# Kernel optimization log

Measured on AMD Instinct MI355X. Metric: run time of the kernel, lower is better.

The kernel has to match this reference:

```python
import jax, jax.numpy as jnp
import numpy as np

N = 100000   # nodes
E = 1600000  # edges
D = 128      # state_dim
H1 = 512
H2 = 256


def setup_inputs() -> dict:
    key = jax.random.key(0)
    ks = jax.random.split(key, 8)
    x = jax.random.normal(ks[0], (N, D), jnp.float32)
    edge_index = jax.random.randint(ks[1], (2, E), 0, N, dtype=jnp.int64)
    W_gcn = jax.random.normal(ks[2], (D, D), jnp.float32) * (1.0 / np.sqrt(D))
    b_gcn = jnp.zeros((D,), jnp.float32)
    W1 = jax.random.normal(ks[3], (D, H1), jnp.float32) * (1.0 / np.sqrt(D))
    b1 = jnp.zeros((H1,), jnp.float32)
    W2 = jax.random.normal(ks[4], (H1, H2), jnp.float32) * (1.0 / np.sqrt(H1))
    b2 = jnp.zeros((H2,), jnp.float32)
    W3 = jax.random.normal(ks[5], (H2, 1), jnp.float32) * (1.0 / np.sqrt(H2))
    b3 = jnp.zeros((1,), jnp.float32)
    return {"x": x, "edge_index": edge_index, "W_gcn": W_gcn, "b_gcn": b_gcn,
            "W1": W1, "b1": b1, "W2": W2, "b2": b2, "W3": W3, "b3": b3}


def _gcn_conv(x, edge_index, W, b):
    # PyG GCNConv: linear transform, add self-loops, symmetric deg^-1/2 norm,
    # scatter-sum messages from src to dst, add bias.
    n = x.shape[0]
    loop = jnp.arange(n, dtype=edge_index.dtype)
    src = jnp.concatenate([edge_index[0], loop])
    dst = jnp.concatenate([edge_index[1], loop])
    deg = jax.ops.segment_sum(jnp.ones_like(dst, x.dtype), dst, num_segments=n)
    dinv = jnp.where(deg > 0, jax.lax.rsqrt(jnp.maximum(deg, 1e-12)), 0.0)
    norm = dinv[src] * dinv[dst]                      # [E+N]
    h = x @ W                                         # [N, D]
    msg = h[src] * norm[:, None]                      # gather + scale
    out = jax.ops.segment_sum(msg, dst, num_segments=n)  # scatter-add
    return out + b


def reference(x, edge_index, W_gcn, b_gcn, W1, b1, W2, b2, W3, b3):
    out = jax.nn.relu(_gcn_conv(x, edge_index, W_gcn, b_gcn))
    h = out + x                                       # residual
    h = jax.nn.relu(h @ W1 + b1)
    h = jax.nn.relu(h @ W2 + b2)                      # dropout is identity in eval
    return h @ W3 + b3                                # [N, 1]
```

## Files before the change

kernel.cpp:

```cpp
#include <hip/hip_runtime.h>

#define DN  128
#define H1N 512
#define H2N 256
#define TILE_A 4096
#define BKT_CAP 6144

typedef __attribute__((ext_vector_type(8))) short short8_t;
typedef __attribute__((ext_vector_type(4))) float f32x4;

__device__ inline ushort f2bf(float f) {
  union { float f; unsigned u; } v; v.f = f;
  unsigned r = v.u + 0x7FFF + ((v.u >> 16) & 1);
  return (ushort)(r >> 16);
}
__device__ inline float asf(unsigned u) {
  union { unsigned u; float f; } v; v.u = u;
  return v.f;
}


__global__ __launch_bounds__(256) void k_bucketA(const int* __restrict__ ei,
                                                 int* __restrict__ bcur,
                                                 uint* __restrict__ pairs,
                                                 int E, int NB) {
  __shared__ int hist[512];
  __shared__ int start[512];
  __shared__ int cur[512];
  __shared__ int gbase[512];
  __shared__ uint lp[TILE_A];
  __shared__ ushort bid[TILE_A];
  int t = threadIdx.x;
  int base = blockIdx.x * TILE_A;
  int cnt = E - base; if (cnt > TILE_A) cnt = TILE_A;

  for (int i = t; i < 512; i += 256) hist[i] = 0;
  __syncthreads();

  int sreg[16], dreg[16];
#pragma unroll
  for (int k = 0; k < 16; ++k) {
    int idx = t + 256 * k;
    bool v = idx < cnt;
    sreg[k] = v ? ei[base + idx] : 0;
    dreg[k] = v ? ei[E + base + idx] : -1;
    if (v) atomicAdd(&hist[dreg[k] >> 8], 1);
  }
  __syncthreads();

  for (int i = t; i < 512; i += 256) start[i] = hist[i];
  __syncthreads();
  for (int o = 1; o < 512; o <<= 1) {
    int i0 = t, i1 = t + 256;
    int v0 = (i0 >= o) ? start[i0 - o] : 0;
    int v1 = (i1 >= o) ? start[i1 - o] : 0;
    __syncthreads();
    start[i0] += v0;
    start[i1] += v1;
    __syncthreads();
  }
  for (int i = t; i < 512; i += 256) start[i] -= hist[i];
  __syncthreads();
  for (int i = t; i < 512; i += 256) cur[i] = start[i];
  __syncthreads();

#pragma unroll
  for (int k = 0; k < 16; ++k) {
    if (dreg[k] >= 0) {
      int d = dreg[k] >> 8;
      int p = atomicAdd(&cur[d], 1);
      lp[p]  = ((uint)sreg[k] << 8) | ((uint)dreg[k] & 255u);
      bid[p] = (ushort)d;
    }
  }
  __syncthreads();

  for (int i = t; i < NB; i += 256)
    gbase[i] = hist[i] ? atomicAdd(&bcur[i], hist[i]) : 0;
  __syncthreads();

  for (int p = t; p < cnt; p += 256) {
    int d = bid[p];
    int o = gbase[d] + (p - start[d]);
    if (o < BKT_CAP) pairs[(size_t)d * BKT_CAP + o] = lp[p];
  }
}


__global__ __launch_bounds__(256) void k_bucketB(const uint* __restrict__ pairs,
                                                 const int* __restrict__ bcur,
                                                 int* __restrict__ csr,
                                                 int* __restrict__ ro,
                                                 int* __restrict__ re,
                                                 float* __restrict__ dinv,
                                                 int N) {
  __shared__ int hist[256];
  __shared__ int cur[256];
  __shared__ int lout[BKT_CAP];
  __shared__ uint lp[BKT_CAP];
  int b = blockIdx.x, t = threadIdx.x;
  size_t p0 = (size_t)b * BKT_CAP;
  int cnt = bcur[b]; if (cnt > BKT_CAP) cnt = BKT_CAP;

  hist[t] = 0;
  __syncthreads();
  for (int k = t; k < cnt; k += 256) {
    uint pr = pairs[p0 + k];
    lp[k] = pr;
    atomicAdd(&hist[pr & 255u], 1);
  }
  __syncthreads();

  int v = hist[t];
  cur[t] = v; __syncthreads();
  for (int o = 1; o < 256; o <<= 1) {
    int a = (t >= o) ? cur[t - o] : 0;
    __syncthreads();
    cur[t] += a;
    __syncthreads();
  }
  int excl = cur[t] - v;
  int node = (b << 8) + t;
  if (node < N) {
    ro[node] = (int)p0 + excl;
    re[node] = (int)p0 + excl + v;
    dinv[node] = rsqrtf((float)(v + 1));
  }
  __syncthreads();
  cur[t] = excl;
  __syncthreads();

  for (int k = t; k < cnt; k += 256) {
    uint pr = lp[k];
    int p = atomicAdd(&cur[(int)(pr & 255u)], 1);
    lout[p] = (int)(pr >> 8);
  }
  __syncthreads();
  for (int k = t; k < cnt; k += 256) csr[p0 + k] = lout[k];
}


__device__ inline void pack_one(int idx, const float* __restrict__ W,
                                ushort* __restrict__ Wp, int K, int Ncols) {
  int ksn = K >> 5;
  int l  = idx & 63;
  int ks = (idx >> 6) % ksn;
  int ct = idx / (64 * ksn);
  int col = ct * 16 + (l & 15);
  int kb  = ks * 32 + (l >> 4) * 8;
  short8_t v;
#pragma unroll
  for (int r = 0; r < 8; ++r)
    v[r] = (short)f2bf(W[(size_t)(kb + r) * Ncols + col]);
  *(short8_t*)&Wp[(size_t)idx * 8] = v;
}

__global__ __launch_bounds__(256) void k_packall(const float* __restrict__ Wg,
                                                 const float* __restrict__ W1,
                                                 const float* __restrict__ W2,
                                                 ushort* __restrict__ Wgp,
                                                 ushort* __restrict__ W1p,
                                                 ushort* __restrict__ W2p) {
  int idx = blockIdx.x * 256 + threadIdx.x;
  if (idx < 2048)        pack_one(idx, Wg, Wgp, DN, DN);
  else if (idx < 10240)  pack_one(idx - 2048, W1, W1p, DN, H1N);
  else if (idx < 26624)  pack_one(idx - 10240, W2, W2p, H1N, H2N);
}


__global__ __launch_bounds__(256, 4) void k_gemm1(const float* __restrict__ x,
                                                  const ushort* __restrict__ Wgp,
                                                  const float* __restrict__ dinv,
                                                  ushort* __restrict__ hs,
                                                  ushort* __restrict__ xb, int N) {
  __shared__ ushort xT[64 * 128];
  int t = threadIdx.x;
  int row0 = blockIdx.x * 64;

#pragma unroll
  for (int i = 0; i < 4; ++i) {
    int c = t + 256 * i;
    int r = c >> 4, d0 = (c & 15) * 8;
    int gr = row0 + r;
    float4 v0 = {0,0,0,0}, v1 = {0,0,0,0};
    if (gr < N) {
      v0 = *(const float4*)(x + (size_t)gr * DN + d0);
      v1 = *(const float4*)(x + (size_t)gr * DN + d0 + 4);
    }
    short8_t p;
    p[0]=(short)f2bf(v0.x); p[1]=(short)f2bf(v0.y); p[2]=(short)f2bf(v0.z); p[3]=(short)f2bf(v0.w);
    p[4]=(short)f2bf(v1.x); p[5]=(short)f2bf(v1.y); p[6]=(short)f2bf(v1.z); p[7]=(short)f2bf(v1.w);
    if (gr < N) {
      int s = (c & 15) >> 1, half = (c & 15) & 1;
      *(short8_t*)(xb + ((size_t)s * N + gr) * 16 + half * 8) = p;
    }
    *(short8_t*)((char*)xT + r * 256 + ((d0 * 2) ^ ((r & 7) << 4))) = p;
  }
  __syncthreads();

  int w = t >> 6, l = t & 63;
  int lr = l & 15, lk = l >> 4;
  const short8_t* pbg = (const short8_t*)Wgp;

  f32x4 acc[4][2];
#pragma unroll
  for (int mf = 0; mf < 4; ++mf)
#pragma unroll
    for (int n = 0; n < 2; ++n) acc[mf][n] = (f32x4){0.f,0.f,0.f,0.f};

  auto g_load = [&](short8_t (&bb)[2], int ks) {
#pragma unroll
    for (int n = 0; n < 2; ++n)
      bb[n] = pbg[((w * 2 + n) * 4 + ks) * 64 + l];
  };
  auto g_mfma = [&](short8_t (&bb)[2], int ks) {
    short8_t a[4];
#pragma unroll
    for (int mf = 0; mf < 4; ++mf) {
      int r = mf * 16 + lr;
      a[mf] = *(const short8_t*)((const char*)xT + r * 256 + ((ks * 64 + lk * 16) ^ ((r & 7) << 4)));
    }
#pragma unroll
    for (int mf = 0; mf < 4; ++mf)
#pragma unroll
      for (int n = 0; n < 2; ++n)
        acc[mf][n] = __builtin_amdgcn_mfma_f32_16x16x32_bf16(a[mf], bb[n], acc[mf][n], 0, 0, 0);
  };

  short8_t bA[2], bB[2];
  g_load(bA, 0);
  g_load(bB, 1); g_mfma(bA, 0);
  g_load(bA, 2); g_mfma(bB, 1);
  g_load(bB, 3); g_mfma(bA, 2);
  g_mfma(bB, 3);

  float dv[4][4];
#pragma unroll
  for (int mf = 0; mf < 4; ++mf)
#pragma unroll
    for (int r2 = 0; r2 < 4; ++r2) {
      int gr = row0 + mf * 16 + lk * 4 + r2;
      dv[mf][r2] = (gr < N) ? dinv[gr] : 0.f;
    }
#pragma unroll
  for (int n = 0; n < 2; ++n) {
    int s = w * 2 + n;
#pragma unroll
    for (int mf = 0; mf < 4; ++mf)
#pragma unroll
      for (int r2 = 0; r2 < 4; ++r2) {
        int gr = row0 + mf * 16 + lk * 4 + r2;
        if (gr < N)
          hs[((size_t)s * N + gr) * 16 + lr] = f2bf(acc[mf][n][r2] * dv[mf][r2]);
      }
  }
}


__global__ __launch_bounds__(256) void k_agg(const ushort* __restrict__ hs,
                                             const ushort* __restrict__ xb,
                                             const int* __restrict__ csr,
                                             const int* __restrict__ ro,
                                             const int* __restrict__ re,
                                             const float* __restrict__ dinv,
                                             const float* __restrict__ bg,
                                             ushort* __restrict__ aggb, int N) {
  int t = threadIdx.x;
  int slice = blockIdx.x & 7;
  int node = (blockIdx.x >> 3) * 64 + (t >> 2);
  if (node >= N) return;
  int d0 = (t & 3) * 4;

  const ushort* hss = hs + (size_t)slice * N * 16;
  int beg = ro[node], end = re[node];
  float dn = dinv[node];
  uint2 selfv = *(const uint2*)(hss + (size_t)node * 16 + d0);
  uint2 xv    = *(const uint2*)(xb + ((size_t)slice * N + node) * 16 + d0);
  float4 bv   = *(const float4*)(bg + slice * 16 + d0);

  float s0 = 0.f, s1 = 0.f, s2 = 0.f, s3 = 0.f;
  auto accum = [&](uint2 v) {
    s0 += asf(v.x << 16); s1 += asf(v.x & 0xffff0000u);
    s2 += asf(v.y << 16); s3 += asf(v.y & 0xffff0000u);
  };

  int e = beg;
  for (; e + 4 <= end; e += 4) {
    int i0 = csr[e], i1 = csr[e + 1], i2 = csr[e + 2], i3 = csr[e + 3];
    uint2 v0 = *(const uint2*)(hss + (size_t)i0 * 16 + d0);
    uint2 v1 = *(const uint2*)(hss + (size_t)i1 * 16 + d0);
    uint2 v2 = *(const uint2*)(hss + (size_t)i2 * 16 + d0);
    uint2 v3 = *(const uint2*)(hss + (size_t)i3 * 16 + d0);
    accum(v0); accum(v1); accum(v2); accum(v3);
  }
  if (e + 2 <= end) {
    int i0 = csr[e], i1 = csr[e + 1];
    uint2 v0 = *(const uint2*)(hss + (size_t)i0 * 16 + d0);
    uint2 v1 = *(const uint2*)(hss + (size_t)i1 * 16 + d0);
    accum(v0); accum(v1);
    e += 2;
  }
  if (e < end) {
    int i0 = csr[e];
    accum(*(const uint2*)(hss + (size_t)i0 * 16 + d0));
  }
  accum(selfv);

  uint outp[2];
  {
    ushort lo = f2bf(fmaxf(s0 * dn + bv.x, 0.f) + asf(xv.x << 16));
    ushort hi = f2bf(fmaxf(s1 * dn + bv.y, 0.f) + asf(xv.x & 0xffff0000u));
    outp[0] = (uint)lo | ((uint)hi << 16);
    lo = f2bf(fmaxf(s2 * dn + bv.z, 0.f) + asf(xv.y << 16));
    hi = f2bf(fmaxf(s3 * dn + bv.w, 0.f) + asf(xv.y & 0xffff0000u));
    outp[1] = (uint)lo | ((uint)hi << 16);
  }
  *(uint2*)(aggb + ((size_t)slice * N + node) * 16 + d0) = *(uint2*)outp;
}


__global__ __launch_bounds__(512, 2) void k_mlp(const ushort* __restrict__ aggb,
                                                const ushort* __restrict__ W1p,
                                                const float* __restrict__ b1,
                                                const ushort* __restrict__ W2p,
                                                const float* __restrict__ b2,
                                                const float* __restrict__ W3,
                                                const float* __restrict__ b3,
                                                float* __restrict__ out, int N) {
  __shared__ ushort aT[64 * 128];
  __shared__ ushort t1[64 * 512];
  int t = threadIdx.x;
  int row0 = blockIdx.x * 64;

#pragma unroll
  for (int i = 0; i < 2; ++i) {
    int u = t + 512 * i;
    int slice = u >> 7;
    int v = u & 127;
    int r = v >> 1, half = v & 1;
    int gr = row0 + r;
    uint4 val = {0, 0, 0, 0};
    if (gr < N) val = *(const uint4*)(aggb + ((size_t)slice * N + gr) * 16 + half * 8);
    int d0 = slice * 16 + half * 8;
    *(uint4*)((char*)aT + r * 256 + ((d0 * 2) ^ ((r & 7) << 4))) = val;
  }
  __syncthreads();

  int w = t >> 6, l = t & 63;
  int lr = l & 15, lk = l >> 4;

  const short8_t* pb1 = (const short8_t*)W1p;
  f32x4 acc1[4][4];
#pragma unroll
  for (int mf = 0; mf < 4; ++mf)
#pragma unroll
    for (int n = 0; n < 4; ++n) acc1[mf][n] = (f32x4){0.f,0.f,0.f,0.f};

  auto s1_load = [&](short8_t (&bb)[4], int ks) {
#pragma unroll
    for (int n = 0; n < 4; ++n)
      bb[n] = pb1[((w * 4 + n) * 4 + ks) * 64 + l];
  };
  auto s1_mfma = [&](short8_t (&bb)[4], int ks) {
    short8_t a[4];
#pragma unroll
    for (int mf = 0; mf < 4; ++mf) {
      int r = mf * 16 + lr;
      a[mf] = *(const short8_t*)((const char*)aT + r * 256 + ((ks * 64 + lk * 16) ^ ((r & 7) << 4)));
    }
#pragma unroll
    for (int mf = 0; mf < 4; ++mf)
#pragma unroll
      for (int n = 0; n < 4; ++n)
        acc1[mf][n] = __builtin_amdgcn_mfma_f32_16x16x32_bf16(a[mf], bb[n], acc1[mf][n], 0, 0, 0);
  };

  {
    short8_t bA[4], bB[4];
    s1_load(bA, 0);
    s1_load(bB, 1); s1_mfma(bA, 0);
    s1_load(bA, 2); s1_mfma(bB, 1);
    s1_load(bB, 3); s1_mfma(bA, 2);
    s1_mfma(bB, 3);
  }

#pragma unroll
  for (int n = 0; n < 4; ++n) {
    int col = (w * 4 + n) * 16 + lr;
    float bb = b1[col];
#pragma unroll
    for (int mf = 0; mf < 4; ++mf)
#pragma unroll
      for (int r2 = 0; r2 < 4; ++r2) {
        int rr = mf * 16 + lk * 4 + r2;
        *(ushort*)((char*)t1 + rr * 1024 + ((col * 2) ^ ((rr & 7) << 4))) =
            f2bf(fmaxf(acc1[mf][n][r2] + bb, 0.f));
      }
  }
  __syncthreads();

  const short8_t* pb2 = (const short8_t*)W2p;
  f32x4 acc2[4][2];
#pragma unroll
  for (int mf = 0; mf < 4; ++mf)
#pragma unroll
    for (int n = 0; n < 2; ++n) acc2[mf][n] = (f32x4){0.f,0.f,0.f,0.f};

  auto s2_load = [&](short8_t (&bb)[4], int p) {
#pragma unroll
    for (int n = 0; n < 2; ++n) {
      bb[n]     = pb2[((w * 2 + n) * 16 + 2 * p)     * 64 + l];
      bb[2 + n] = pb2[((w * 2 + n) * 16 + 2 * p + 1) * 64 + l];
    }
  };
  auto s2_mfma = [&](short8_t (&bb)[4], int p) {
#pragma unroll
    for (int h = 0; h < 2; ++h) {
      int ks = 2 * p + h;
      short8_t a[4];
#pragma unroll
      for (int mf = 0; mf < 4; ++mf) {
        int r = mf * 16 + lr;
        a[mf] = *(const short8_t*)((const char*)t1 + r * 1024 + ((ks * 64 + lk * 16) ^ ((r & 7) << 4)));
      }
#pragma unroll
      for (int mf = 0; mf < 4; ++mf)
#pragma unroll
        for (int n = 0; n < 2; ++n)
          acc2[mf][n] = __builtin_amdgcn_mfma_f32_16x16x32_bf16(a[mf], bb[2 * h + n], acc2[mf][n], 0, 0, 0);
    }
  };

  {
    short8_t c0[4], c1[4], c2[4];
    s2_load(c0, 0); s2_load(c1, 1);
    s2_load(c2, 2); s2_mfma(c0, 0);
    s2_load(c0, 3); s2_mfma(c1, 1);
    s2_load(c1, 4); s2_mfma(c2, 2);
    s2_load(c2, 5); s2_mfma(c0, 3);
    s2_load(c0, 6); s2_mfma(c1, 4);
    s2_load(c1, 7); s2_mfma(c2, 5);
    s2_mfma(c0, 6);
    s2_mfma(c1, 7);
  }

  float po[4][4];
#pragma unroll
  for (int mf = 0; mf < 4; ++mf)
#pragma unroll
    for (int r2 = 0; r2 < 4; ++r2) po[mf][r2] = 0.f;
#pragma unroll
  for (int n = 0; n < 2; ++n) {
    int col = (w * 2 + n) * 16 + lr;
    float bb = b2[col];
    float w3 = W3[col];
#pragma unroll
    for (int mf = 0; mf < 4; ++mf)
#pragma unroll
      for (int r2 = 0; r2 < 4; ++r2)
        po[mf][r2] += fmaxf(acc2[mf][n][r2] + bb, 0.f) * w3;
  }
#pragma unroll
  for (int mf = 0; mf < 4; ++mf)
#pragma unroll
    for (int r2 = 0; r2 < 4; ++r2) {
      float v = po[mf][r2];
      v += __shfl_xor(v, 1, 64);
      v += __shfl_xor(v, 2, 64);
      v += __shfl_xor(v, 4, 64);
      v += __shfl_xor(v, 8, 64);
      po[mf][r2] = v;
    }
  float* pf = (float*)aT;
  if (lr == 0) {
#pragma unroll
    for (int mf = 0; mf < 4; ++mf)
#pragma unroll
      for (int r2 = 0; r2 < 4; ++r2)
        pf[w * 64 + mf * 16 + lk * 4 + r2] = po[mf][r2];
  }
  __syncthreads();
  if (t < 64) {
    int gr = row0 + t;
    if (gr < N) {
      float s = b3[0];
#pragma unroll
      for (int ww = 0; ww < 8; ++ww) s += pf[ww * 64 + t];
      out[gr] = s;
    }
  }
}


extern "C" void kernel_launch(void* const* d_in, const int* in_sizes, int n_in,
                              void* d_out, int out_size, void* d_ws, size_t ws_size,
                              hipStream_t stream) {
  const float* x  = (const float*)d_in[0];
  const int*   ei = (const int*)d_in[1];
  const float* Wg = (const float*)d_in[2];
  const float* bg = (const float*)d_in[3];
  const float* W1 = (const float*)d_in[4];
  const float* b1 = (const float*)d_in[5];
  const float* W2 = (const float*)d_in[6];
  const float* b2 = (const float*)d_in[7];
  const float* W3 = (const float*)d_in[8];
  const float* b3 = (const float*)d_in[9];
  float* out = (float*)d_out;

  const int N = in_sizes[0] / DN;
  const int E = in_sizes[1] / 2;
  const int NB = (N + 255) >> 8;

  char* ws = (char*)d_ws;
  size_t off = 0;
  auto alloc = [&](size_t bytes) -> void* {
    void* p = ws + off;
    off = (off + bytes + 255) & ~(size_t)255;
    return p;
  };
  int*    bcur   = (int*)alloc((size_t)NB * 4);
  int*    ro     = (int*)alloc((size_t)N * 4);
  int*    re     = (int*)alloc((size_t)N * 4);
  float*  dinv   = (float*)alloc((size_t)N * 4);
  int*    csr    = (int*)alloc((size_t)NB * BKT_CAP * 4);
  uint*   pairs  = (uint*)alloc((size_t)NB * BKT_CAP * 4);
  ushort* hsb    = (ushort*)alloc((size_t)N * DN * 2);
  ushort* aggb   = (ushort*)alloc((size_t)N * DN * 2);
  ushort* xbb    = (ushort*)alloc((size_t)N * DN * 2);
  ushort* Wgp    = (ushort*)alloc((size_t)DN * DN * 2);
  ushort* W1p    = (ushort*)alloc((size_t)DN * H1N * 2);
  ushort* W2p    = (ushort*)alloc((size_t)H1N * H2N * 2);
  (void)ws_size; (void)n_in; (void)out_size;

  hipMemsetAsync(bcur, 0, (size_t)NB * 4, stream);

  int nTiles = (E + TILE_A - 1) / TILE_A;
  k_bucketA<<<nTiles, 256, 0, stream>>>(ei, bcur, pairs, E, NB);
  k_bucketB<<<NB, 256, 0, stream>>>(pairs, bcur, csr, ro, re, dinv, N);

  k_packall<<<104, 256, 0, stream>>>(Wg, W1, W2, Wgp, W1p, W2p);

  int nb64 = (N + 63) / 64;
  k_gemm1<<<nb64, 256, 0, stream>>>(x, Wgp, dinv, hsb, xbb, N);
  k_agg<<<nb64 * 8, 256, 0, stream>>>(hsb, xbb, csr, ro, re, dinv, bg, aggb, N);
  k_mlp<<<nb64, 512, 0, stream>>>(aggb, W1p, b1, W2p, b2, W3, b3, out, N);
}
```

Baseline: 214.1 us.

## Drop bf16 x copy, widen aggregation gathers to 16 bytes, deepen MLP weight prefetch

The GEMM1 kernel no longer writes a sliced bf16 copy of x. The aggregation kernel now reads the fp32 residual straight from x, which removes one write and one read pass of a 25 MB buffer. Each aggregation thread now handles 8 features with 16-byte gathers, so 2 lanes share a node instead of 4 and each block covers 128 nodes. The MLP stages also prefetch one more weight fragment ahead, at the cost of extra registers. The residual add now uses full fp32 x rather than bf16, which changes numerics slightly.

Result: slower. 222.5 us (+3.9%).

```diff
diff --git a/kernel.cpp b/kernel.cpp
--- a/kernel.cpp
+++ b/kernel.cpp
@@ -171,8 +171,7 @@
 __global__ __launch_bounds__(256, 4) void k_gemm1(const float* __restrict__ x,
                                                   const ushort* __restrict__ Wgp,
                                                   const float* __restrict__ dinv,
-                                                  ushort* __restrict__ hs,
-                                                  ushort* __restrict__ xb, int N) {
+                                                  ushort* __restrict__ hs, int N) {
   __shared__ ushort xT[64 * 128];
   int t = threadIdx.x;
   int row0 = blockIdx.x * 64;
@@ -190,10 +189,6 @@
     short8_t p;
     p[0]=(short)f2bf(v0.x); p[1]=(short)f2bf(v0.y); p[2]=(short)f2bf(v0.z); p[3]=(short)f2bf(v0.w);
     p[4]=(short)f2bf(v1.x); p[5]=(short)f2bf(v1.y); p[6]=(short)f2bf(v1.z); p[7]=(short)f2bf(v1.w);
-    if (gr < N) {
-      int s = (c & 15) >> 1, half = (c & 15) & 1;
-      *(short8_t*)(xb + ((size_t)s * N + gr) * 16 + half * 8) = p;
-    }
     *(short8_t*)((char*)xT + r * 256 + ((d0 * 2) ^ ((r & 7) << 4))) = p;
   }
   __syncthreads();
@@ -258,7 +253,7 @@
 
 
 __global__ __launch_bounds__(256) void k_agg(const ushort* __restrict__ hs,
-                                             const ushort* __restrict__ xb,
+                                             const float* __restrict__ x,
                                              const int* __restrict__ csr,
                                              const int* __restrict__ ro,
                                              const int* __restrict__ re,
@@ -267,55 +262,62 @@
                                              ushort* __restrict__ aggb, int N) {
   int t = threadIdx.x;
   int slice = blockIdx.x & 7;
-  int node = (blockIdx.x >> 3) * 64 + (t >> 2);
+  int node = (blockIdx.x >> 3) * 128 + (t >> 1);
   if (node >= N) return;
-  int d0 = (t & 3) * 4;
+  int d0 = (t & 1) * 8;
 
   const ushort* hss = hs + (size_t)slice * N * 16;
   int beg = ro[node], end = re[node];
   float dn = dinv[node];
-  uint2 selfv = *(const uint2*)(hss + (size_t)node * 16 + d0);
-  uint2 xv    = *(const uint2*)(xb + ((size_t)slice * N + node) * 16 + d0);
-  float4 bv   = *(const float4*)(bg + slice * 16 + d0);
-
-  float s0 = 0.f, s1 = 0.f, s2 = 0.f, s3 = 0.f;
-  auto accum = [&](uint2 v) {
-    s0 += asf(v.x << 16); s1 += asf(v.x & 0xffff0000u);
-    s2 += asf(v.y << 16); s3 += asf(v.y & 0xffff0000u);
+  uint4 selfv = *(const uint4*)(hss + (size_t)node * 16 + d0);
+  float4 x0 = *(const float4*)(x + (size_t)node * DN + slice * 16 + d0);
+  float4 x1 = *(const float4*)(x + (size_t)node * DN + slice * 16 + d0 + 4);
+  float4 b0 = *(const float4*)(bg + slice * 16 + d0);
+  float4 b1v = *(const float4*)(bg + slice * 16 + d0 + 4);
+
+  float s[8];
+#pragma unroll
+  for (int i = 0; i < 8; ++i) s[i] = 0.f;
+
+  auto accum = [&](uint4 v) {
+    s[0] += asf(v.x << 16); s[1] += asf(v.x & 0xffff0000u);
+    s[2] += asf(v.y << 16); s[3] += asf(v.y & 0xffff0000u);
+    s[4] += asf(v.z << 16); s[5] += asf(v.z & 0xffff0000u);
+    s[6] += asf(v.w << 16); s[7] += asf(v.w & 0xffff0000u);
   };
 
   int e = beg;
   for (; e + 4 <= end; e += 4) {
     int i0 = csr[e], i1 = csr[e + 1], i2 = csr[e + 2], i3 = csr[e + 3];
-    uint2 v0 = *(const uint2*)(hss + (size_t)i0 * 16 + d0);
-    uint2 v1 = *(const uint2*)(hss + (size_t)i1 * 16 + d0);
-    uint2 v2 = *(const uint2*)(hss + (size_t)i2 * 16 + d0);
-    uint2 v3 = *(const uint2*)(hss + (size_t)i3 * 16 + d0);
+    uint4 v0 = *(const uint4*)(hss + (size_t)i0 * 16 + d0);
+    uint4 v1 = *(const uint4*)(hss + (size_t)i1 * 16 + d0);
+    uint4 v2 = *(const uint4*)(hss + (size_t)i2 * 16 + d0);
+    uint4 v3 = *(const uint4*)(hss + (size_t)i3 * 16 + d0);
     accum(v0); accum(v1); accum(v2); accum(v3);
   }
   if (e + 2 <= end) {
     int i0 = csr[e], i1 = csr[e + 1];
-    uint2 v0 = *(const uint2*)(hss + (size_t)i0 * 16 + d0);
-    uint2 v1 = *(const uint2*)(hss + (size_t)i1 * 16 + d0);
+    uint4 v0 = *(const uint4*)(hss + (size_t)i0 * 16 + d0);
+    uint4 v1 = *(const uint4*)(hss + (size_t)i1 * 16 + d0);
     accum(v0); accum(v1);
     e += 2;
   }
   if (e < end) {
     int i0 = csr[e];
-    accum(*(const uint2*)(hss + (size_t)i0 * 16 + d0));
+    accum(*(const uint4*)(hss + (size_t)i0 * 16 + d0));
   }
   accum(selfv);
 
-  uint outp[2];
-  {
-    ushort lo = f2bf(fmaxf(s0 * dn + bv.x, 0.f) + asf(xv.x << 16));
-    ushort hi = f2bf(fmaxf(s1 * dn + bv.y, 0.f) + asf(xv.x & 0xffff0000u));
-    outp[0] = (uint)lo | ((uint)hi << 16);
-    lo = f2bf(fmaxf(s2 * dn + bv.z, 0.f) + asf(xv.y << 16));
-    hi = f2bf(fmaxf(s3 * dn + bv.w, 0.f) + asf(xv.y & 0xffff0000u));
-    outp[1] = (uint)lo | ((uint)hi << 16);
-  }
-  *(uint2*)(aggb + ((size_t)slice * N + node) * 16 + d0) = *(uint2*)outp;
+  float xv[8] = {x0.x, x0.y, x0.z, x0.w, x1.x, x1.y, x1.z, x1.w};
+  float bv[8] = {b0.x, b0.y, b0.z, b0.w, b1v.x, b1v.y, b1v.z, b1v.w};
+  uint outp[4];
+#pragma unroll
+  for (int i = 0; i < 4; ++i) {
+    ushort lo = f2bf(fmaxf(s[2*i]   * dn + bv[2*i],   0.f) + xv[2*i]);
+    ushort hi = f2bf(fmaxf(s[2*i+1] * dn + bv[2*i+1], 0.f) + xv[2*i+1]);
+    outp[i] = (uint)lo | ((uint)hi << 16);
+  }
+  *(uint4*)(aggb + ((size_t)slice * N + node) * 16 + d0) = *(uint4*)outp;
 }
 
 
@@ -376,12 +378,12 @@
   };
 
   {
-    short8_t bA[4], bB[4];
-    s1_load(bA, 0);
-    s1_load(bB, 1); s1_mfma(bA, 0);
-    s1_load(bA, 2); s1_mfma(bB, 1);
-    s1_load(bB, 3); s1_mfma(bA, 2);
-    s1_mfma(bB, 3);
+    short8_t bA[4], bB[4], bC[4];
+    s1_load(bA, 0); s1_load(bB, 1); s1_load(bC, 2);
+    s1_mfma(bA, 0); s1_load(bA, 3);
+    s1_mfma(bB, 1);
+    s1_mfma(bC, 2);
+    s1_mfma(bA, 3);
   }
 
 #pragma unroll
@@ -432,16 +434,16 @@
   };
 
   {
-    short8_t c0[4], c1[4], c2[4];
-    s2_load(c0, 0); s2_load(c1, 1);
-    s2_load(c2, 2); s2_mfma(c0, 0);
-    s2_load(c0, 3); s2_mfma(c1, 1);
-    s2_load(c1, 4); s2_mfma(c2, 2);
-    s2_load(c2, 5); s2_mfma(c0, 3);
-    s2_load(c0, 6); s2_mfma(c1, 4);
-    s2_load(c1, 7); s2_mfma(c2, 5);
-    s2_mfma(c0, 6);
-    s2_mfma(c1, 7);
+    short8_t c0[4], c1[4], c2b[4], c3[4];
+    s2_load(c0, 0); s2_load(c1, 1); s2_load(c2b, 2);
+    s2_load(c3, 3); s2_mfma(c0, 0);
+    s2_load(c0, 4); s2_mfma(c1, 1);
+    s2_load(c1, 5); s2_mfma(c2b, 2);
+    s2_load(c2b, 6); s2_mfma(c3, 3);
+    s2_load(c3, 7); s2_mfma(c0, 4);
+    s2_mfma(c1, 5);
+    s2_mfma(c2b, 6);
+    s2_mfma(c3, 7);
   }
 
   float po[4][4];
@@ -526,7 +528,6 @@
   uint*   pairs  = (uint*)alloc((size_t)NB * BKT_CAP * 4);
   ushort* hsb    = (ushort*)alloc((size_t)N * DN * 2);
   ushort* aggb   = (ushort*)alloc((size_t)N * DN * 2);
-  ushort* xbb    = (ushort*)alloc((size_t)N * DN * 2);
   ushort* Wgp    = (ushort*)alloc((size_t)DN * DN * 2);
   ushort* W1p    = (ushort*)alloc((size_t)DN * H1N * 2);
   ushort* W2p    = (ushort*)alloc((size_t)H1N * H2N * 2);
@@ -541,7 +542,8 @@
   k_packall<<<104, 256, 0, stream>>>(Wg, W1, W2, Wgp, W1p, W2p);
 
   int nb64 = (N + 63) / 64;
-  k_gemm1<<<nb64, 256, 0, stream>>>(x, Wgp, dinv, hsb, xbb, N);
-  k_agg<<<nb64 * 8, 256, 0, stream>>>(hsb, xbb, csr, ro, re, dinv, bg, aggb, N);
+  k_gemm1<<<nb64, 256, 0, stream>>>(x, Wgp, dinv, hsb, N);
+  int nb128 = (N + 127) / 128;
+  k_agg<<<nb128 * 8, 256, 0, stream>>>(hsb, x, csr, ro, re, dinv, bg, aggb, N);
   k_mlp<<<nb64, 512, 0, stream>>>(aggb, W1p, b1, W2p, b2, W3, b3, out, N);
 }
```
